# Kernel tuning notes

Hardware: AMD Instinct MI355X
Metric: run time of the kernel (lower is better)

## Reference

```python
import jax, jax.numpy as jnp
import numpy as np

EPS = 1e-7
T_NCE = 0.07      # opt.nce_t
MOMENTUM = 0.5    # opt.nce_m
N_DATA = 100000   # opt.n_data


def l2norm(x):
    # Normalize(power=2): x / (sum(x^2, dim=1))^(1/2)
    return x / jnp.sqrt(jnp.sum(x * x, axis=1, keepdims=True))


def contrast_loss(x, P):
    # ContrastLoss (Eq 18). x: [B, P+K] of normalized exp-similarities.
    B, PK = x.shape
    N = PK - P
    m_pn = N * (1.0 / N_DATA)  # m * Pn
    pos = x[:, :P]                                   # [B, P]
    log_D1 = jnp.log(pos / (pos + m_pn + EPS))
    neg = x[:, P:]                                   # [B, N]
    log_D0 = jnp.log(m_pn / (neg + m_pn + EPS))
    # log_D0.view(-1,1).repeat(1,P).sum(0) == P copies of log_D0.sum()
    return -((log_D1.sum(0) + log_D0.sum()) / B).sum() / P


def setup_inputs() -> dict:
    key = jax.random.key(0)
    ks = jax.random.split(key, 10)
    B, S_DIM, T_DIM, FEAT = 64, 2048, 2048, 128
    P, K = 4, 8192
    NCLS, PER = 7, 1000
    stdv = 1.0 / np.sqrt(FEAT / 3.0)
    return {
        "f_s": jax.random.normal(ks[0], (B, S_DIM), jnp.float32),
        "f_t": jax.random.normal(ks[1], (B, T_DIM), jnp.float32),
        "idx": jax.random.randint(ks[2], (B,), 0, N_DATA),
        "batch_label": jax.random.uniform(ks[3], (B, NCLS), dtype=jnp.float32),
        "class_index": jax.random.randint(ks[4], (NCLS, PER), 0, N_DATA),
        "num_pos": P,
        "contrast_idx": jax.random.randint(ks[5], (B, P + K), 0, N_DATA),
        "W_s": jax.random.normal(ks[6], (S_DIM, FEAT), jnp.float32) * 0.02,
        "b_s": jnp.zeros((FEAT,), jnp.float32),
        "W_t": jax.random.normal(ks[7], (T_DIM, FEAT), jnp.float32) * 0.02,
        "b_t": jnp.zeros((FEAT,), jnp.float32),
        "memory_s": jax.random.uniform(ks[8], (N_DATA, FEAT), jnp.float32, -stdv, stdv),
        "memory_t": jax.random.uniform(ks[9], (N_DATA, FEAT), jnp.float32, -stdv, stdv),
    }


def reference(f_s, f_t, idx, batch_label, class_index, num_pos, contrast_idx,
              W_s, b_s, W_t, b_t, memory_s, memory_t):
    # Embed + L2 norm
    f_s = l2norm(f_s @ W_s + b_s)   # [B, D]
    f_t = l2norm(f_t @ W_t + b_t)   # [B, D]

    # ContrastMemory (memory banks are buffers -> no grad through them)
    mem_s = jax.lax.stop_gradient(memory_s)
    mem_t = jax.lax.stop_gradient(memory_t)

    w_t = mem_t[contrast_idx]                                     # [B, P+K, D]
    out_s = jnp.exp(jnp.einsum('bkd,bd->bk', w_t, f_s) / T_NCE)
    out_s = out_s / (jnp.mean(out_s) * N_DATA)                    # Z_s normalization
    w_s = mem_s[contrast_idx]                                     # [B, P+K, D]
    out_t = jnp.exp(jnp.einsum('bkd,bd->bk', w_s, f_t) / T_NCE)
    out_t = out_t / (jnp.mean(out_t) * N_DATA)                    # Z_t normalization

    # momentum memory update (done under no_grad in torch)
    upd_s = l2norm(mem_s[idx] * MOMENTUM + jax.lax.stop_gradient(f_s) * (1.0 - MOMENTUM))
    new_mem_s = mem_s.at[idx].set(upd_s)
    upd_t = l2norm(mem_t[idx] * MOMENTUM + jax.lax.stop_gradient(f_t) * (1.0 - MOMENTUM))
    new_mem_t = mem_t.at[idx].set(upd_t)

    CCD_loss = contrast_loss(out_s, num_pos) + contrast_loss(out_t, num_pos)

    # class-center anchors: gather per-class memory rows, relu, mean -> [NCLS, D]
    s_anchors = l2norm(jnp.mean(jax.nn.relu(new_mem_s[class_index]), axis=1))
    t_anchors = l2norm(jnp.mean(jax.nn.relu(new_mem_t[class_index]), axis=1))

    # anchor relation loss (anchors detached; teacher relation fully detached)
    s_rel = (f_s @ jax.lax.stop_gradient(s_anchors).T) / T_NCE    # [B, NCLS]
    t_rel = jax.lax.stop_gradient((f_t @ t_anchors.T) / T_NCE)
    targets = jax.nn.softmax(t_rel, axis=1)
    log_inputs = jax.nn.log_softmax(s_rel, axis=1)
    relation_loss = jnp.sum(targets * (jnp.log(targets + EPS * 0 + 1e-30) - log_inputs)) / s_rel.shape[0]

    return (CCD_loss, relation_loss, f_s, f_t)
```

## Files before the change

### kernel.cpp

```cpp
#include <hip/hip_runtime.h>
#include <math.h>
#include <stdint.h>

#define B 64
#define SDIM 2048
#define FEAT 128
#define P 4
#define PK 8196
#define NCLS 7
#define PER 1000
#define NDATA 100000
#define EPSC 1e-7f
#define M_PN 0.08192f
#define JCHUNKS 50
#define CS (PER / JCHUNKS)

#define DTBF ((size_t)B * NDATA / 2)
#define KSPLIT 4
#define KSEG 2049
#define KS1 8
#define TPW 2
#define ROWS_BLK (TPW * 16)

#define TILE 16
#define WCHUNK 512
#define NT (WCHUNK / TILE)

#define GLL16(gp, lp) \
    __builtin_amdgcn_global_load_lds( \
        (__attribute__((address_space(1))) void*)(uintptr_t)(gp), \
        (__attribute__((address_space(3))) void*)(lp), 16, 0, 0)

typedef __attribute__((ext_vector_type(8))) short bf16x8;
typedef __attribute__((ext_vector_type(4))) float f32x4;

static __device__ __forceinline__ short f2bf(float x)
{
    union { float f; uint32_t u; } v; v.f = x;
    const uint32_t r = (v.u + 0x7fffu + ((v.u >> 16) & 1u)) >> 16;
    return (short)r;
}
static __device__ __forceinline__ float bf2f(unsigned short u)
{
    union { uint32_t u; float f; } v; v.u = ((uint32_t)u) << 16;
    return v.f;
}

__global__ void gemm_partial_kernel(const float* __restrict__ f_s,
                                    const float* __restrict__ f_t,
                                    const float* __restrict__ W_s,
                                    const float* __restrict__ W_t,
                                    float* __restrict__ fbp)
{
    const int row = blockIdx.x;
    const int z   = blockIdx.y;
    const int ks  = blockIdx.z;
    const float* f = z == 0 ? f_s : f_t;
    const float* W = z == 0 ? W_s : W_t;

    const int t  = threadIdx.x;
    const int d  = t & 127;
    const int kh = t >> 7;

    __shared__ float frow[SDIM / KS1];
    frow[t] = f[row * SDIM + ks * (SDIM / KS1) + t];
    __syncthreads();

    float acc = 0.0f;
    const int kb = ks * (SDIM / KS1) + kh * 128;
    #pragma unroll 8
    for (int k = 0; k < 128; ++k)
        acc = fmaf(frow[kh * 128 + k], W[(kb + k) * FEAT + d], acc);

    __shared__ float part[2][128];
    part[kh][d] = acc;
    __syncthreads();
    if (t < 128)
        fbp[(((size_t)ks * 2 + z) * B + row) * FEAT + t] = part[0][t] + part[1][t];
}

__global__ void norm_finish_kernel(const float* __restrict__ fbp,
                                   const float* __restrict__ b_s,
                                   const float* __restrict__ b_t,
                                   const int*   __restrict__ idx,
                                   const float* __restrict__ mem_s,
                                   const float* __restrict__ mem_t,
                                   float* __restrict__ out_fs,
                                   float* __restrict__ out_ft,
                                   unsigned short* __restrict__ fsb,
                                   unsigned short* __restrict__ ftb,
                                   float* __restrict__ upd)
{
    const int row = blockIdx.x;
    const int z   = blockIdx.y;
    const int d   = threadIdx.x;
    const float* bias = z == 0 ? b_s : b_t;
    float* out = z == 0 ? out_fs : out_ft;
    unsigned short* fbx = z == 0 ? fsb : ftb;

    float a = bias[d];
    #pragma unroll
    for (int ks = 0; ks < KS1; ++ks)
        a += fbp[(((size_t)ks * 2 + z) * B + row) * FEAT + d];

    __shared__ float red[128];
    red[d] = a * a;
    __syncthreads();
    for (int s = 64; s > 0; s >>= 1) {
        if (d < s) red[d] += red[d + s];
        __syncthreads();
    }
    const float v = a * (1.0f / sqrtf(red[0]));
    out[row * FEAT + d] = v;
    fbx[row * FEAT + d] = (unsigned short)f2bf(v);
    __syncthreads();

    const float* mem = z == 0 ? mem_s : mem_t;
    const int i = idx[row];
    const float u = mem[(size_t)i * FEAT + d] * 0.5f + v * 0.5f;
    red[d] = u * u;
    __syncthreads();
    for (int s = 64; s > 0; s >>= 1) {
        if (d < s) red[d] += red[d + s];
        __syncthreads();
    }
    upd[((size_t)z * B + row) * FEAT + d] = u * (1.0f / sqrtf(red[0]));
}

#define MFMA4(av, kc, a0, a1, a2, a3) do { \
    a0 = __builtin_amdgcn_mfma_f32_16x16x32_bf16(av, bv[kc][0], a0, 0, 0, 0); \
    a1 = __builtin_amdgcn_mfma_f32_16x16x32_bf16(av, bv[kc][1], a1, 0, 0, 0); \
    a2 = __builtin_amdgcn_mfma_f32_16x16x32_bf16(av, bv[kc][2], a2, 0, 0, 0); \
    a3 = __builtin_amdgcn_mfma_f32_16x16x32_bf16(av, bv[kc][3], a3, 0, 0, 0); \
    } while (0)

__global__ __launch_bounds__(64)
void dgemm10_kernel(const unsigned short* __restrict__ fsb,
                    const unsigned short* __restrict__ ftb,
                    const float* __restrict__ mem_s,
                    const float* __restrict__ mem_t,
                    short* __restrict__ DT0,
                    short* __restrict__ DT1)
{
    const int z = blockIdx.y;
    const unsigned short* fWb = z == 0 ? fsb : ftb;
    const float* mem          = z == 0 ? mem_t : mem_s;
    short* DT                 = z == 0 ? DT0 : DT1;

    const int l   = threadIdx.x;
    const int ln  = l & 15;
    const int ko  = l >> 4;
    const int xk  = ln & 7;
    const int wrowbase = blockIdx.x * ROWS_BLK;

    __shared__ __align__(16) float rows[2][16 * FEAT];

#define STG(tt, bf) do { \
    _Pragma("unroll") \
    for (int p_ = 0; p_ < 8; ++p_) { \
        const int r_ = 2 * p_ + (l >> 5); \
        int gr_ = wrowbase + (tt) * 16 + r_; \
        if (gr_ >= NDATA) gr_ = NDATA - 1; \
        const float* g_ = mem + (size_t)gr_ * FEAT + (((l & 31) ^ (r_ & 7)) << 2); \
        GLL16(g_, &rows[bf][p_ * 256]); \
    } } while (0)

#define STORE_BF(cc, nt) do { \
    short4 s_; \
    s_.x = f2bf((cc).x); s_.y = f2bf((cc).y); \
    s_.z = f2bf((cc).z); s_.w = f2bf((cc).w); \
    *(short4*)(DT + (size_t)((nt) * 16 + ln) * NDATA + growb) = s_; \
    } while (0)

#define COMPUTE_STORE(t_, buf_) do { \
    const float* rb = &rows[buf_][ln * FEAT]; \
    f32x4 c0 = (f32x4){0.f,0.f,0.f,0.f}; \
    f32x4 c1 = (f32x4){0.f,0.f,0.f,0.f}; \
    f32x4 c2 = (f32x4){0.f,0.f,0.f,0.f}; \
    f32x4 c3 = (f32x4){0.f,0.f,0.f,0.f}; \
    _Pragma("unroll") \
    for (int kc = 0; kc < 4; ++kc) { \
        const int g0 = kc * 8 + ko * 2; \
        const float4 lo = *(const float4*)(rb + (((g0 + 0) ^ xk) << 2)); \
        const float4 hi = *(const float4*)(rb + (((g0 + 1) ^ xk) << 2)); \
        const bf16x8 av = (bf16x8){ f2bf(lo.x), f2bf(lo.y), f2bf(lo.z), f2bf(lo.w), \
                                    f2bf(hi.x), f2bf(hi.y), f2bf(hi.z), f2bf(hi.w) }; \
        MFMA4(av, kc, c0, c1, c2, c3); \
    } \
    const int growb = wrowbase + (t_) * 16 + ko * 4; \
    if (growb < NDATA) { \
        STORE_BF(c0, 0); \
        STORE_BF(c1, 1); \
        STORE_BF(c2, 2); \
        STORE_BF(c3, 3); \
    } } while (0)

    STG(0, 0);
    STG(1, 1);

    bf16x8 bv[4][4];
    #pragma unroll
    for (int kc = 0; kc < 4; ++kc)
        #pragma unroll
        for (int nt = 0; nt < 4; ++nt)
            bv[kc][nt] = *(const bf16x8*)(fWb + (nt * 16 + ln) * FEAT + kc * 32 + ko * 8);

    asm volatile("s_waitcnt vmcnt(8)" ::: "memory");
    __builtin_amdgcn_sched_barrier(0);
    COMPUTE_STORE(0, 0);

    asm volatile("s_waitcnt vmcnt(4)" ::: "memory");
    __builtin_amdgcn_sched_barrier(0);
    COMPUTE_STORE(1, 1);

#undef STG
#undef STORE_BF
#undef COMPUTE_STORE
}

__global__ void gather2_kernel(const int* __restrict__ contrast_idx,
                               const unsigned short* __restrict__ DT0,
                               const unsigned short* __restrict__ DT1,
                               float* __restrict__ out_raw,
                               float* __restrict__ Ssum)
{
    const int z   = blockIdx.z;
    const int b   = blockIdx.y;
    const int ks  = blockIdx.x;
    const int tid = threadIdx.x;
    const int k0  = ks * KSEG;
    const int kend = min(k0 + KSEG, PK);
    const float inv_t = 1.0f / 0.07f;
    const unsigned short* dtb = (z == 0 ? DT0 : DT1) + (size_t)b * NDATA;
    float* orz = out_raw + (size_t)z * (B * PK);
    float lsum = 0.0f;
    #pragma unroll 4
    for (int k = k0 + tid; k < kend; k += 256) {
        const int ci = contrast_idx[(size_t)b * PK + k];
        const float v = expf(bf2f(dtb[ci]) * inv_t);
        orz[(size_t)b * PK + k] = v;
        lsum += v;
    }
    __shared__ float red[256];
    red[tid] = lsum;
    __syncthreads();
    for (int s = 128; s > 0; s >>= 1) {
        if (tid < s) red[tid] += red[tid + s];
        __syncthreads();
    }
    if (tid == 0) atomicAdd(&Ssum[z], red[0]);
}

__global__ void ccd_loss_kernel(const float* __restrict__ out_raw,
                                const float* __restrict__ Ssum,
                                float* __restrict__ acc)
{
    const int z = blockIdx.y;
    const float S = Ssum[z];
    const float c = ((float)(B * PK)) / (S * (float)NDATA);

    const int total = B * PK;
    float contrib = 0.0f;
    for (int i = blockIdx.x * blockDim.x + threadIdx.x; i < total;
         i += gridDim.x * blockDim.x) {
        const float v = out_raw[(size_t)z * total + i] * c;
        const int k = i % PK;
        if (k < P) {
            contrib += logf(v / (v + M_PN + EPSC));
        } else {
            contrib += (float)P * logf(M_PN / (v + M_PN + EPSC));
        }
    }
    __shared__ float red[256];
    red[threadIdx.x] = contrib;
    __syncthreads();
    for (int s = 128; s > 0; s >>= 1) {
        if (threadIdx.x < s) red[threadIdx.x] += red[threadIdx.x + s];
        __syncthreads();
    }
    if (threadIdx.x == 0) atomicAdd(&acc[z], red[0]);
}

__global__ void gemm_norm_kernel(const float* __restrict__ f_s,
                                 const float* __restrict__ f_t,
                                 const float* __restrict__ W_s,
                                 const float* __restrict__ b_s,
                                 const float* __restrict__ W_t,
                                 const float* __restrict__ b_t,
                                 float* __restrict__ out_fs,
                                 float* __restrict__ out_ft)
{
    const int row = blockIdx.x;
    const int z   = blockIdx.y;
    const float* f    = z == 0 ? f_s : f_t;
    const float* W    = z == 0 ? W_s : W_t;
    const float* bias = z == 0 ? b_s : b_t;
    float* out        = z == 0 ? out_fs : out_ft;

    __shared__ __align__(16) float frow[SDIM];
    const int t  = threadIdx.x;
    const int d  = t & 127;
    const int kh = t >> 7;
    for (int k = t; k < SDIM; k += 256) frow[k] = f[row * SDIM + k];
    __syncthreads();

    float acc = 0.0f;
    const int k0 = kh * (SDIM / 2);
    for (int k = k0; k < k0 + SDIM / 2; ++k)
        acc = fmaf(frow[k], W[k * FEAT + d], acc);

    __shared__ float part[2][128];
    part[kh][d] = acc;
    __syncthreads();
    const float a = part[0][d] + part[1][d] + bias[d];

    __shared__ float red[256];
    red[t] = (t < 128) ? a * a : 0.0f;
    __syncthreads();
    for (int s = 128; s > 0; s >>= 1) {
        if (t < s) red[t] += red[t + s];
        __syncthreads();
    }
    if (t < 128) out[row * FEAT + t] = a * (1.0f / sqrtf(red[0]));
}

__global__ __launch_bounds__(64)
void dots_kernel(const float* __restrict__ fsn,
                 const float* __restrict__ ftn,
                 const int*   __restrict__ contrast_idx,
                 const float* __restrict__ mem_s,
                 const float* __restrict__ mem_t,
                 float* __restrict__ out_raw,
                 float* __restrict__ Ssum)
{
    const int z = blockIdx.z;
    const int b = blockIdx.y;
    const int l = threadIdx.x;
    const int kchunk = blockIdx.x * WCHUNK;

    const float* f   = (z == 0 ? fsn : ftn) + b * FEAT;
    const float* mem = (z == 0 ? mem_t : mem_s);

    __shared__ __align__(16) float rows[2][TILE * FEAT];
    __shared__ __align__(16) float fl[FEAT];
    __shared__ int cis[WCHUNK];

    fl[l]      = f[l];
    fl[l + 64] = f[l + 64];
    for (int i = l; i < WCHUNK; i += 64) {
        const int k = kchunk + i;
        cis[i] = contrast_idx[(size_t)b * PK + (k < PK ? k : PK - 1)];
    }
    __syncthreads();

    const int q   = l >> 4;
    const int r_c = l & 15;
    const int xk  = r_c & 7;
    const int rh  = l >> 5;
    const int sl  = l & 31;

    const float4* fg = (const float4*)fl;
    const float4 f0 = fg[q * 8 + 0], f1 = fg[q * 8 + 1];
    const float4 f2 = fg[q * 8 + 2], f3 = fg[q * 8 + 3];
    const float4 f4 = fg[q * 8 + 4], f5 = fg[q * 8 + 5];
    const float4 f6 = fg[q * 8 + 6], f7 = fg[q * 8 + 7];

    const float inv_t = 1.0f / 0.07f;
    const size_t obase = (size_t)z * (B * PK) + (size_t)b * PK;
    float lsum = 0.0f;

#define STAGE(tt, bf) do { \
    _Pragma("unroll") \
    for (int p_ = 0; p_ < 8; ++p_) { \
        const int rr_ = 2 * p_ + rh; \
        const int ci_ = cis[(tt) * TILE + rr_]; \
        const float* g_ = mem + (size_t)ci_ * FEAT + ((sl ^ (rr_ & 7)) << 2); \
        GLL16(g_, &rows[bf][p_ * 256]); \
    } } while (0)

    STAGE(0, 0);
    int cur = 0;
    for (int t = 0; t < NT; ++t) {
        if (t + 1 < NT) {
            STAGE(t + 1, cur ^ 1);
            asm volatile("s_waitcnt vmcnt(8)" ::: "memory");
        } else {
            asm volatile("s_waitcnt vmcnt(0)" ::: "memory");
        }
        __builtin_amdgcn_sched_barrier(0);

        const float* rbase = &rows[cur][r_c * FEAT];
        float dot;
        {
            const float4 m0 = *(const float4*)(rbase + (((q * 8 + 0) ^ xk) << 2));
            const float4 m1 = *(const float4*)(rbase + (((q * 8 + 1) ^ xk) << 2));
            const float4 m2 = *(const float4*)(rbase + (((q * 8 + 2) ^ xk) << 2));
            const float4 m3 = *(const float4*)(rbase + (((q * 8 + 3) ^ xk) << 2));
            const float4 m4 = *(const float4*)(rbase + (((q * 8 + 4) ^ xk) << 2));
            const float4 m5 = *(const float4*)(rbase + (((q * 8 + 5) ^ xk) << 2));
            const float4 m6 = *(const float4*)(rbase + (((q * 8 + 6) ^ xk) << 2));
            const float4 m7 = *(const float4*)(rbase + (((q * 8 + 7) ^ xk) << 2));
            dot = m0.x * f0.x;
            dot = fmaf(m0.y, f0.y, dot); dot = fmaf(m0.z, f0.z, dot); dot = fmaf(m0.w, f0.w, dot);
            dot = fmaf(m1.x, f1.x, dot); dot = fmaf(m1.y, f1.y, dot); dot = fmaf(m1.z, f1.z, dot); dot = fmaf(m1.w, f1.w, dot);
            dot = fmaf(m2.x, f2.x, dot); dot = fmaf(m2.y, f2.y, dot); dot = fmaf(m2.z, f2.z, dot); dot = fmaf(m2.w, f2.w, dot);
            dot = fmaf(m3.x, f3.x, dot); dot = fmaf(m3.y, f3.y, dot); dot = fmaf(m3.z, f3.z, dot); dot = fmaf(m3.w, f3.w, dot);
            dot = fmaf(m4.x, f4.x, dot); dot = fmaf(m4.y, f4.y, dot); dot = fmaf(m4.z, f4.z, dot); dot = fmaf(m4.w, f4.w, dot);
            dot = fmaf(m5.x, f5.x, dot); dot = fmaf(m5.y, f5.y, dot); dot = fmaf(m5.z, f5.z, dot); dot = fmaf(m5.w, f5.w, dot);
            dot = fmaf(m6.x, f6.x, dot); dot = fmaf(m6.y, f6.y, dot); dot = fmaf(m6.z, f6.z, dot); dot = fmaf(m6.w, f6.w, dot);
            dot = fmaf(m7.x, f7.x, dot); dot = fmaf(m7.y, f7.y, dot); dot = fmaf(m7.z, f7.z, dot); dot = fmaf(m7.w, f7.w, dot);
        }
        dot += __shfl_xor(dot, 16);
        dot += __shfl_xor(dot, 32);

        const int krow = kchunk + t * TILE + r_c;
        if (q == 0 && krow < PK) {
            const float val = expf(dot * inv_t);
            out_raw[obase + krow] = val;
            lsum += val;
        }
        cur ^= 1;
    }
#undef STAGE

    lsum += __shfl_xor(lsum, 8);
    lsum += __shfl_xor(lsum, 4);
    lsum += __shfl_xor(lsum, 2);
    lsum += __shfl_xor(lsum, 1);
    if (l == 0) atomicAdd(&Ssum[z], lsum);
}

__global__ void upd_kernel(const float* __restrict__ fsn,
                           const float* __restrict__ ftn,
                           const int*   __restrict__ idx,
                           const float* __restrict__ mem_s,
                           const float* __restrict__ mem_t,
                           float* __restrict__ upd)
{
    const int z = blockIdx.y;
    const int b = blockIdx.x;
    const int d = threadIdx.x;
    const float* mem = z == 0 ? mem_s : mem_t;
    const float* f   = z == 0 ? fsn : ftn;
    const int i = idx[b];
    const float v = mem[(size_t)i * FEAT + d] * 0.5f + f[b * FEAT + d] * 0.5f;
    __shared__ float red[128];
    red[d] = v * v;
    __syncthreads();
    for (int s = 64; s > 0; s >>= 1) {
        if (d < s) red[d] += red[d + s];
        __syncthreads();
    }
    upd[(size_t)z * (B * FEAT) + b * FEAT + d] = v * (1.0f / sqrtf(red[0]));
}

__global__ void anchors_partial2_kernel(const int* __restrict__ class_index,
                                        const int* __restrict__ idx,
                                        const float* __restrict__ mem_s,
                                        const float* __restrict__ mem_t,
                                        const float* __restrict__ upd,
                                        float* __restrict__ partial)
{
    const int z     = blockIdx.z;
    const int c     = blockIdx.y;
    const int chunk = blockIdx.x;
    const int d     = threadIdx.x;
    const float* mem = z == 0 ? mem_s : mem_t;
    const float* u   = upd + (size_t)z * (B * FEAT);

    __shared__ int lidx[B];
    __shared__ int cis[CS];
    __shared__ int rbs[CS];
    if (d < B) lidx[d] = idx[d];
    __syncthreads();
    if (d < CS) {
        const int e = c * PER + chunk * CS + d;
        const int ci = class_index[e];
        int rb = -1;
        for (int b = B - 1; b >= 0; --b) {
            if (lidx[b] == ci) { rb = b; break; }
        }
        cis[d] = ci;
        rbs[d] = rb;
    }
    __syncthreads();

    float acc = 0.0f;
    #pragma unroll 4
    for (int j = 0; j < CS; ++j) {
        const int ci = cis[j];
        const int rb = rbs[j];
        const float* row = (rb >= 0) ? (u + rb * FEAT) : (mem + (size_t)ci * FEAT);
        const float v = row[d];
        acc += v > 0.0f ? v : 0.0f;
    }
    atomicAdd(&partial[(size_t)z * (NCLS * FEAT) + c * FEAT + d], acc);
}

__global__ void final2_kernel(const float* __restrict__ fsn,
                              const float* __restrict__ ftn,
                              const float* __restrict__ partial,
                              const float* __restrict__ acc,
                              float* __restrict__ d_out)
{
    __shared__ float an[2 * NCLS * FEAT];
    __shared__ float red[128];
    const int tid = threadIdx.x;

    for (int zc = 0; zc < 2 * NCLS; ++zc) {
        const float mv = partial[(size_t)zc * FEAT + tid] * (1.0f / (float)PER);
        red[tid] = mv * mv;
        __syncthreads();
        for (int s = 64; s > 0; s >>= 1) {
            if (tid < s) red[tid] += red[tid + s];
            __syncthreads();
        }
        an[zc * FEAT + tid] = mv * (1.0f / sqrtf(red[0]));
        __syncthreads();
    }

    float contrib = 0.0f;
    if (tid < 64) {
        const int b = tid;
        const float* sa = an;
        const float* ta = an + NCLS * FEAT;
        float srel[NCLS], trel[NCLS];
        for (int j = 0; j < NCLS; ++j) { srel[j] = 0.0f; trel[j] = 0.0f; }
        for (int d = 0; d < FEAT; ++d) {
            const float fs = fsn[b * FEAT + d];
            const float ft = ftn[b * FEAT + d];
            #pragma unroll
            for (int j = 0; j < NCLS; ++j) {
                srel[j] = fmaf(fs, sa[j * FEAT + d], srel[j]);
                trel[j] = fmaf(ft, ta[j * FEAT + d], trel[j]);
            }
        }
        const float inv_t = 1.0f / 0.07f;
        float smax = -1e30f, tmax = -1e30f;
        for (int j = 0; j < NCLS; ++j) {
            srel[j] *= inv_t; trel[j] *= inv_t;
            smax = fmaxf(smax, srel[j]);
            tmax = fmaxf(tmax, trel[j]);
        }
        float ssum = 0.0f, tsum = 0.0f;
        float texp[NCLS];
        for (int j = 0; j < NCLS; ++j) {
            ssum += expf(srel[j] - smax);
            texp[j] = expf(trel[j] - tmax);
            tsum += texp[j];
        }
        const float lse_s = logf(ssum);
        for (int j = 0; j < NCLS; ++j) {
            const float tgt = texp[j] / tsum;
            const float log_in = srel[j] - smax - lse_s;
            contrib += tgt * (logf(tgt + 1e-30f) - log_in);
        }
        for (int off = 32; off > 0; off >>= 1) contrib += __shfl_down(contrib, off);
        if (tid == 0) {
            d_out[1] = contrib / (float)B;
            d_out[0] = -(acc[0] + acc[1]) / (float)(B * P);
        }
    }
}

extern "C" void kernel_launch(void* const* d_in, const int* in_sizes, int n_in,
                              void* d_out_v, int out_size, void* d_ws, size_t ws_size,
                              hipStream_t stream)
{
    const float* f_s = (const float*)d_in[0];
    const float* f_t = (const float*)d_in[1];
    const int*   idx = (const int*)d_in[2];
    const int*   class_index = (const int*)d_in[4];
    const int*   contrast_idx = (const int*)d_in[6];
    const float* W_s = (const float*)d_in[7];
    const float* b_s = (const float*)d_in[8];
    const float* W_t = (const float*)d_in[9];
    const float* b_t = (const float*)d_in[10];
    const float* mem_s = (const float*)d_in[11];
    const float* mem_t = (const float*)d_in[12];

    float* out    = (float*)d_out_v;
    float* out_fs = out + 2;
    float* out_ft = out + 2 + B * FEAT;

    float* ws = (float*)d_ws;
    const size_t fl = ws_size / sizeof(float);
    const size_t REST = 2 * (size_t)B * PK
                      + (size_t)B * FEAT
                      + (size_t)KS1 * 2 * B * FEAT
                      + 2 * B * FEAT
                      + 2 * NCLS * FEAT
                      + 64;
    const bool fit = fl >= 2 * DTBF + REST;

    if (fit) {
        short* DT0 = (short*)ws;
        short* DT1 = (short*)(ws + DTBF);
        float* p   = ws + 2 * DTBF;
        float* out_raw = p;            p += 2 * (size_t)B * PK;
        unsigned short* fsb = (unsigned short*)p;  p += B * FEAT / 2;
        unsigned short* ftb = (unsigned short*)p;  p += B * FEAT / 2;
        float* fbp     = p;            p += (size_t)KS1 * 2 * B * FEAT;
        float* upd     = p;            p += 2 * B * FEAT;
        float* partial = p;            p += 2 * NCLS * FEAT;
        float* Ssum    = p;            p += 2;
        float* acc     = p;            p += 2;

        hipMemsetAsync(partial, 0, (2 * NCLS * FEAT + 4) * sizeof(float), stream);

        dim3 g1a(B, 2, KS1);
        gemm_partial_kernel<<<g1a, 256, 0, stream>>>(f_s, f_t, W_s, W_t, fbp);
        dim3 g1b(B, 2);
        norm_finish_kernel<<<g1b, 128, 0, stream>>>(fbp, b_s, b_t, idx,
                                                    mem_s, mem_t,
                                                    out_fs, out_ft, fsb, ftb, upd);

        const int gblocks = (NDATA + ROWS_BLK - 1) / ROWS_BLK;
        dim3 gd(gblocks, 2);
        dgemm10_kernel<<<gd, 64, 0, stream>>>(fsb, ftb, mem_s, mem_t,
                                              DT0, DT1);
        dim3 gg(KSPLIT, B, 2);
        gather2_kernel<<<gg, 256, 0, stream>>>(contrast_idx,
                                               (const unsigned short*)DT0,
                                               (const unsigned short*)DT1,
                                               out_raw, Ssum);

        dim3 g3(256, 2);
        ccd_loss_kernel<<<g3, 256, 0, stream>>>(out_raw, Ssum, acc);
        dim3 g5a(JCHUNKS, NCLS, 2);
        anchors_partial2_kernel<<<g5a, 128, 0, stream>>>(class_index, idx,
                                                         mem_s, mem_t, upd, partial);
        final2_kernel<<<1, 128, 0, stream>>>(out_fs, out_ft, partial, acc, out);
    } else {
        float* out_raw = ws;
        float* upd     = out_raw + 2 * (B * PK);
        float* partial = upd + 2 * (B * FEAT);
        float* Ssum    = partial + 2 * (NCLS * FEAT);
        float* acc     = Ssum + 2;

        hipMemsetAsync(partial, 0, (2 * NCLS * FEAT + 4) * sizeof(float), stream);

        dim3 g1(B, 2);
        gemm_norm_kernel<<<g1, 256, 0, stream>>>(f_s, f_t, W_s, b_s, W_t, b_t,
                                                 out_fs, out_ft);
        dim3 g2((PK + WCHUNK - 1) / WCHUNK, B, 2);
        dots_kernel<<<g2, 64, 0, stream>>>(out_fs, out_ft, contrast_idx,
                                           mem_s, mem_t, out_raw, Ssum);
        dim3 g3(256, 2);
        ccd_loss_kernel<<<g3, 256, 0, stream>>>(out_raw, Ssum, acc);
        dim3 g4(B, 2);
        upd_kernel<<<g4, 128, 0, stream>>>(out_fs, out_ft, idx, mem_s, mem_t, upd);
        dim3 g5a(JCHUNKS, NCLS, 2);
        anchors_partial2_kernel<<<g5a, 128, 0, stream>>>(class_index, idx,
                                                         mem_s, mem_t, upd, partial);
        final2_kernel<<<1, 128, 0, stream>>>(out_fs, out_ft, partial, acc, out);
    }
}
```

Before: 112.2 us.

## Fuse contrast gather and CCD loss into one cooperative kernel

Replaces the separate gather kernel (which wrote exp-similarities to a global buffer) and the CCD loss kernel with a single cooperative-launch kernel. Each thread keeps its up to nine gathered values in registers, a grid-wide sync waits for the global normalization sum, and the loss is then computed in place. This removes the global round trip for the out_raw buffer and one kernel launch. In exchange it needs a cooperative launch of 512 blocks that must all be resident at once, and it pays for a grid barrier.

Measured after the change: 189.3 us. 68.7% more time.

```diff
diff --git a/kernel.cpp b/kernel.cpp
--- a/kernel.cpp
+++ b/kernel.cpp
@@ -1,6 +1,9 @@
 #include <hip/hip_runtime.h>
+#include <hip/hip_cooperative_groups.h>
 #include <math.h>
 #include <stdint.h>
+
+namespace cg = cooperative_groups;
 
 #define B 64
 #define SDIM 2048
@@ -18,6 +21,7 @@
 #define DTBF ((size_t)B * NDATA / 2)
 #define KSPLIT 4
 #define KSEG 2049
+#define NIT 9
 #define KS1 8
 #define TPW 2
 #define ROWS_BLK (TPW * 16)
@@ -218,6 +222,73 @@
 #undef COMPUTE_STORE
 }
 
+__global__ __launch_bounds__(256)
+void coop_loss_kernel(const int* __restrict__ contrast_idx,
+                      const unsigned short* __restrict__ DT0,
+                      const unsigned short* __restrict__ DT1,
+                      float* __restrict__ Ssum,
+                      float* __restrict__ acc)
+{
+    const int z   = blockIdx.z;
+    const int b   = blockIdx.y;
+    const int ks  = blockIdx.x;
+    const int tid = threadIdx.x;
+    const int k0  = ks * KSEG;
+    const int kend = min(k0 + KSEG, PK);
+    const float inv_t = 1.0f / 0.07f;
+    const unsigned short* dtb = (z == 0 ? DT0 : DT1) + (size_t)b * NDATA;
+
+    float vv0 = 0.f, vv1 = 0.f, vv2 = 0.f, vv3 = 0.f, vv4 = 0.f,
+          vv5 = 0.f, vv6 = 0.f, vv7 = 0.f, vv8 = 0.f;
+    float lsum = 0.0f;
+
+#define GATH(it, dst) do { \
+    const int k = k0 + tid + (it) * 256; \
+    if (k < kend) { \
+        const int ci = contrast_idx[(size_t)b * PK + k]; \
+        dst = expf(bf2f(dtb[ci]) * inv_t); \
+        lsum += dst; \
+    } } while (0)
+    GATH(0, vv0); GATH(1, vv1); GATH(2, vv2); GATH(3, vv3); GATH(4, vv4);
+    GATH(5, vv5); GATH(6, vv6); GATH(7, vv7); GATH(8, vv8);
+#undef GATH
+
+    __shared__ float red[256];
+    red[tid] = lsum;
+    __syncthreads();
+    for (int s = 128; s > 0; s >>= 1) {
+        if (tid < s) red[tid] += red[tid + s];
+        __syncthreads();
+    }
+    if (tid == 0) atomicAdd(&Ssum[z], red[0]);
+
+    cg::this_grid().sync();
+
+    const float S = atomicAdd(&Ssum[z], 0.0f);
+    const float c = ((float)(B * PK)) / (S * (float)NDATA);
+
+    float contrib = 0.0f;
+#define LOSS(it, src) do { \
+    const int k = k0 + tid + (it) * 256; \
+    if (k < kend) { \
+        const float v = (src) * c; \
+        if (k < P) contrib += logf(v / (v + M_PN + EPSC)); \
+        else       contrib += (float)P * logf(M_PN / (v + M_PN + EPSC)); \
+    } } while (0)
+    LOSS(0, vv0); LOSS(1, vv1); LOSS(2, vv2); LOSS(3, vv3); LOSS(4, vv4);
+    LOSS(5, vv5); LOSS(6, vv6); LOSS(7, vv7); LOSS(8, vv8);
+#undef LOSS
+
+    __syncthreads();
+    red[tid] = contrib;
+    __syncthreads();
+    for (int s = 128; s > 0; s >>= 1) {
+        if (tid < s) red[tid] += red[tid + s];
+        __syncthreads();
+    }
+    if (tid == 0) atomicAdd(&acc[z], red[0]);
+}
+
 __global__ void gather2_kernel(const int* __restrict__ contrast_idx,
                                const unsigned short* __restrict__ DT0,
                                const unsigned short* __restrict__ DT1,
@@ -605,6 +676,7 @@
         float* partial = p;            p += 2 * NCLS * FEAT;
         float* Ssum    = p;            p += 2;
         float* acc     = p;            p += 2;
+        (void)out_raw;
 
         hipMemsetAsync(partial, 0, (2 * NCLS * FEAT + 4) * sizeof(float), stream);
 
@@ -619,14 +691,18 @@
         dim3 gd(gblocks, 2);
         dgemm10_kernel<<<gd, 64, 0, stream>>>(fsb, ftb, mem_s, mem_t,
                                               DT0, DT1);
-        dim3 gg(KSPLIT, B, 2);
-        gather2_kernel<<<gg, 256, 0, stream>>>(contrast_idx,
-                                               (const unsigned short*)DT0,
-                                               (const unsigned short*)DT1,
-                                               out_raw, Ssum);
-
-        dim3 g3(256, 2);
-        ccd_loss_kernel<<<g3, 256, 0, stream>>>(out_raw, Ssum, acc);
+
+        {
+            const unsigned short* cDT0 = (const unsigned short*)DT0;
+            const unsigned short* cDT1 = (const unsigned short*)DT1;
+            void* args[] = { (void*)&contrast_idx, (void*)&cDT0, (void*)&cDT1,
+                             (void*)&Ssum, (void*)&acc };
+            dim3 gg(KSPLIT, B, 2);
+            dim3 bb(256, 1, 1);
+            hipLaunchCooperativeKernel((void*)coop_loss_kernel, gg, bb,
+                                       args, 0, stream);
+        }
+
         dim3 g5a(JCHUNKS, NCLS, 2);
         anchors_partial2_kernel<<<g5a, 128, 0, stream>>>(class_index, idx,
                                                          mem_s, mem_t, upd, partial);
```
